# Kernel optimization log

Measured on AMD Instinct MI355X. Metric: run time of the kernel, lower is better.

The kernel has to match this reference:

```python
import jax, jax.numpy as jnp
import numpy as np

B = 262144
MF = 16  # metadata_features
C = 128  # trunk width
EPS = 1e-6


def _linear(x, w, b):
    # torch nn.Linear: y = x @ w.T + b, w shape [out, in]
    return x @ w.T + b


def _adain(x, style):
    # style: [B, 2*C] viewed as [B, C, 2]; [...,0]=scale, [...,1]=bias
    s = style.reshape(x.shape[0], x.shape[1], 2)
    scale, bias = s[:, :, 0], s[:, :, 1]
    mu = jnp.mean(x, axis=-1, keepdims=True)
    # torch.std default is unbiased (ddof=1)
    var = jnp.sum((x - mu) ** 2, axis=-1, keepdims=True) / (x.shape[1] - 1)
    sigma = jnp.sqrt(var) + EPS
    return scale * (x - mu) / sigma + bias


def setup_inputs() -> dict:
    key = jax.random.key(0)
    ks = jax.random.split(key, 20)
    n = jax.random.normal
    d = dict(
        x=n(ks[0], (B, 1), jnp.float32),
        metadata=n(ks[1], (B, MF), jnp.float32),
        # MetadataMLP: MF -> 64 -> 128 -> 1024
        mw1=n(ks[2], (64, MF), jnp.float32) * 0.2,
        mb1=jnp.zeros((64,), jnp.float32),
        mw2=n(ks[3], (128, 64), jnp.float32) * 0.1,
        mb2=jnp.zeros((128,), jnp.float32),
        mw3=n(ks[4], (1024, 128), jnp.float32) * 0.1,
        mb3=jnp.zeros((1024,), jnp.float32),
        # trunk
        w1=n(ks[5], (C, 1), jnp.float32) * 0.5,
        b1=jnp.zeros((C,), jnp.float32),
        w2=n(ks[6], (C, C), jnp.float32) * 0.1,
        b2=jnp.zeros((C,), jnp.float32),
        w3=n(ks[7], (C, C), jnp.float32) * 0.1,
        b3=jnp.zeros((C,), jnp.float32),
        w4=n(ks[8], (C, C), jnp.float32) * 0.1,
        b4=jnp.zeros((C,), jnp.float32),
        w5=n(ks[9], (1, C), jnp.float32) * 0.1,
        b5=jnp.zeros((1,), jnp.float32),
    )
    return d


def reference(x, metadata, mw1, mb1, mw2, mb2, mw3, mb3,
              w1, b1, w2, b2, w3, b3, w4, b4, w5, b5):
    lrelu = lambda v: jax.nn.leaky_relu(v, 0.01)
    # MetadataMLP -> style vectors [B, 1024]
    h = jax.nn.relu(_linear(metadata, mw1, mb1))
    h = jax.nn.relu(_linear(h, mw2, mb2))
    style = _linear(h, mw3, mb3)
    s1, s2, s3, s4 = jnp.split(style, 4, axis=1)  # each [B, 256]

    y = lrelu(_adain(_linear(x, w1, b1), s1))
    y = lrelu(_adain(_linear(y, w2, b2), s2))
    y = lrelu(_adain(_linear(y, w3, b3), s3))
    y = lrelu(_adain(_linear(y, w4, b4), s4))
    out = lrelu(_linear(y, w5, b5))  # [B, 1]
    return out
```

## Files before the change

### kernel.cpp

```cpp
#include <hip/hip_runtime.h>

#define RPB  64
#define NTHR 128

typedef _Float16 f16;
typedef _Float16 f16x4 __attribute__((ext_vector_type(4)));
typedef _Float16 f16x8 __attribute__((ext_vector_type(8)));
typedef float    f32x4 __attribute__((ext_vector_type(4)));

#define G_MW2 1024
#define G_W   2048
#define G_MW3 16384
#define GO_MW2 0
#define GO_W2  (GO_MW2 + G_MW2)
#define GO_W3  (GO_W2 + G_W)
#define GO_W4  (GO_W3 + G_W)
#define GO_MW3 (GO_W4 + G_W)
#define G_TOT  (GO_MW3 + G_MW3)
#define G_MW1Q 256
#define WS_BYTES ((size_t)G_TOT * 16 + (size_t)G_MW1Q * 8)

#define OFF_H2    0
#define OFF_B     17408
#define OFF_H1    (OFF_B)
#define OFF_STATS (OFF_B + 17408)
#define OFF_OUT   (OFF_STATS + 1024)
#define OFF_X     (OFF_OUT + 512)
#define SMEM_SZ   (OFF_X + 256)

__device__ __forceinline__ f16x8 cvt8(const float* __restrict__ p) {
  const float4* p4 = (const float4*)p;
  float4 f0 = p4[0], f1 = p4[1];
  f16x8 o;
  o[0]=(f16)f0.x; o[1]=(f16)f0.y; o[2]=(f16)f0.z; o[3]=(f16)f0.w;
  o[4]=(f16)f1.x; o[5]=(f16)f1.y; o[6]=(f16)f1.z; o[7]=(f16)f1.w;
  return o;
}

__device__ __forceinline__ f16x4 cvt4v(float4 f) {
  f16x4 o;
  o[0]=(f16)f.x; o[1]=(f16)f.y; o[2]=(f16)f.z; o[3]=(f16)f.w;
  return o;
}

__global__ void pack_weights(const float* __restrict__ mw1, const float* __restrict__ mw2,
                             const float* __restrict__ w2,  const float* __restrict__ w3,
                             const float* __restrict__ w4,  const float* __restrict__ mw3,
                             f16x8* __restrict__ ws) {
  int g = blockIdx.x * blockDim.x + threadIdx.x;
  if (g >= G_TOT + G_MW1Q) return;
  if (g >= G_TOT) {
    const int local = g - G_TOT;
    const int lane = local & 63, jt = local >> 6;
    const int j = jt * 16 + (lane & 15);
    const int k0 = (lane >> 4) * 4;
    ((f16x4*)(ws + G_TOT))[local] = cvt4v(*(const float4*)(mw1 + j * 16 + k0));
    return;
  }
  if (g < GO_MW3) {
    const float* W; int K; int local;
    if (g < GO_W2)       { W = mw2; K = 64;  local = g; }
    else if (g < GO_W3)  { W = w2;  K = 128; local = g - GO_W2; }
    else if (g < GO_W4)  { W = w3;  K = 128; local = g - GO_W3; }
    else                 { W = w4;  K = 128; local = g - GO_W4; }
    const int lane = local & 63, fb = local >> 6;
    const int ksteps = K >> 5;
    const int ks = fb % ksteps, n0g = fb / ksteps;
    const int n  = n0g * 16 + (lane & 15);
    const int k0 = ks * 32 + (lane >> 4) * 8;
    ws[g] = cvt8(W + (size_t)n * K + k0);
  } else {
    const int local = g - GO_MW3;
    const int lane = local & 63, fb = local >> 6;
    const int ks = fb & 3, sb = (fb >> 2) & 1, tt = (fb >> 3) & 3;
    const int ch = (fb >> 5) & 1, l = fb >> 6;
    const int n  = l * 256 + 2 * (ch * 64 + tt * 16 + (lane & 15)) + sb;
    const int k0 = ks * 32 + (lane >> 4) * 8;
    ws[g] = cvt8(mw3 + (size_t)n * 128 + k0);
  }
}

template<bool WS>
__device__ __forceinline__ f16x8 ldB(const f16x8* __restrict__ wp,
                                     const float* __restrict__ wf,
                                     int K, int n0, int ks, int lane) {
  if constexpr (WS) {
    return wp[((n0 >> 4) * (K >> 5) + ks) * 64 + lane];
  } else {
    const int n  = n0 + (lane & 15);
    const int k0 = ks * 32 + (lane >> 4) * 8;
    return cvt8(wf + (size_t)n * K + k0);
  }
}

template<bool WS>
__device__ __forceinline__ f16x8 ldB3(const f16x8* __restrict__ wp,
                                      const float* __restrict__ wf,
                                      int l, int ch, int tt, int sb, int ks, int lane) {
  if constexpr (WS) {
    const int fb = (((l * 2 + ch) * 4 + tt) * 2 + sb) * 4 + ks;
    return wp[fb * 64 + lane];
  } else {
    const int n  = l * 256 + 2 * (ch * 64 + tt * 16 + (lane & 15)) + sb;
    const int k0 = ks * 32 + (lane >> 4) * 8;
    return cvt8(wf + (size_t)n * 128 + k0);
  }
}

template<bool WS>
__device__ __forceinline__ f16x4 ldB1(const f16x8* __restrict__ wsp,
                                      const float* __restrict__ mw1f,
                                      int jt, int lane) {
  if constexpr (WS) {
    return ((const f16x4*)(wsp + G_TOT))[jt * 64 + lane];
  } else {
    const int j = jt * 16 + (lane & 15);
    const int k0 = (lane >> 4) * 4;
    return cvt4v(*(const float4*)(mw1f + j * 16 + k0));
  }
}

#define MFMA(a, b, c)   __builtin_amdgcn_mfma_f32_16x16x32_f16((a), (b), (c), 0, 0, 0)
#define MFMA16(a, b, c) __builtin_amdgcn_mfma_f32_16x16x16f16((a), (b), (c), 0, 0, 0)

template<bool WS>
__global__ __launch_bounds__(NTHR, 2)
void adain_mfma(const float* __restrict__ x,   const float* __restrict__ meta,
                const float* __restrict__ mw1, const float* __restrict__ mb1,
                const float* __restrict__ mw2, const float* __restrict__ mb2,
                const float* __restrict__ mw3, const float* __restrict__ mb3,
                const float* __restrict__ w1,  const float* __restrict__ b1,
                const float* __restrict__ w2,  const float* __restrict__ b2,
                const float* __restrict__ w3,  const float* __restrict__ b3,
                const float* __restrict__ w4,  const float* __restrict__ b4,
                const float* __restrict__ w5,  const float* __restrict__ b5,
                const f16x8* __restrict__ wsp, float* __restrict__ out)
{
  __shared__ __align__(16) char smem[SMEM_SZ];
  f16    (*sH2)[136]   = (f16(*)[136])  (smem + OFF_H2);
  f16    (*sH1)[72]    = (f16(*)[72])   (smem + OFF_H1);
  f16    (*sY)[136]    = (f16(*)[136])  (smem + OFF_B);
  float2 (*sStats)[2]  = (float2(*)[2]) (smem + OFF_STATS);
  float  (*sOut)[2]    = (float(*)[2])  (smem + OFF_OUT);
  float  *sX           = (float*)       (smem + OFF_X);

  const int t    = threadIdx.x;
  const int lane = t & 63;
  const int ch   = t >> 6;
  const int r0   = blockIdx.x * RPB;
  const int ln   = lane & 15;
  const int bg   = lane >> 4;
  const int acol = bg * 8;
  const int g4   = bg * 4;

  const f16x8* wsp3 = wsp + GO_MW3;

  if (t < RPB) sX[t] = x[r0 + t];

  {
    f16x4 am[4];
#pragma unroll
    for (int p = 0; p < 4; ++p)
      am[p] = cvt4v(*(const float4*)(meta + (size_t)(r0 + p * 16 + ln) * 16 + g4));
#pragma unroll
    for (int jj = 0; jj < 2; ++jj) {
      const int jt = ch * 2 + jj;
      const f16x4 wj = ldB1<WS>(wsp, mw1, jt, lane);
      const float4 bb = *(const float4*)(mb1 + jt * 16 + g4);
      const f32x4 cini = {bb.x, bb.y, bb.z, bb.w};
#pragma unroll
      for (int p = 0; p < 4; ++p) {
        f32x4 acc = MFMA16(wj, am[p], cini);
        f16x4 hv;
#pragma unroll
        for (int q = 0; q < 4; ++q) hv[q] = (f16)fmaxf(acc[q], 0.0f);
        *(f16x4*)&sH1[p * 16 + ln][jt * 16 + g4] = hv;
      }
    }
  }
  __syncthreads();

  {
    f16x8 a0[4], a1[4];
#pragma unroll
    for (int p = 0; p < 4; ++p) {
      const int ar = p * 16 + ln;
      a0[p] = *(const f16x8*)&sH1[ar][acol];
      a1[p] = *(const f16x8*)&sH1[ar][32 + acol];
    }
#pragma unroll
    for (int tt = 0; tt < 4; ++tt) {
      const int n0 = ch * 64 + tt * 16;
      f16x8 b0 = ldB<WS>(wsp + GO_MW2, mw2, 64, n0, 0, lane);
      f16x8 b1 = ldB<WS>(wsp + GO_MW2, mw2, 64, n0, 1, lane);
      const float4 bb = *(const float4*)(mb2 + n0 + g4);
      const f32x4 cini = {bb.x, bb.y, bb.z, bb.w};
#pragma unroll
      for (int p = 0; p < 4; ++p) {
        f32x4 acc = MFMA(b0, a0[p], cini);
        acc = MFMA(b1, a1[p], acc);
        f16x4 hv;
#pragma unroll
        for (int q = 0; q < 4; ++q) hv[q] = (f16)fmaxf(acc[q], 0.0f);
        *(f16x4*)&sH2[p * 16 + ln][n0 + g4] = hv;
      }
    }
  }
  __syncthreads();

#pragma unroll 1
  for (int l = 0; l < 4; ++l) {
    f32x4 accM[4][4];

    if (l == 0) {
#pragma unroll
      for (int tt = 0; tt < 4; ++tt) {
        const int c4 = ch * 64 + tt * 16 + g4;
        const float4 w1v = *(const float4*)(w1 + c4);
        const float4 b1v = *(const float4*)(b1 + c4);
#pragma unroll
        for (int p = 0; p < 4; ++p) {
          const float xv = sX[p * 16 + ln];
          accM[p][tt][0] = xv * w1v.x + b1v.x;
          accM[p][tt][1] = xv * w1v.y + b1v.y;
          accM[p][tt][2] = xv * w1v.z + b1v.z;
          accM[p][tt][3] = xv * w1v.w + b1v.w;
        }
      }
    } else {
      const f16x8* Wp_ = (l == 1) ? wsp + GO_W2 : (l == 2) ? wsp + GO_W3 : wsp + GO_W4;
      const float* Wf_ = (l == 1) ? w2 : (l == 2) ? w3 : w4;
      const float* Bv_ = (l == 1) ? b2 : (l == 2) ? b3 : b4;
#pragma unroll
      for (int tt = 0; tt < 4; ++tt) {
        const float4 bv = *(const float4*)(Bv_ + ch * 64 + tt * 16 + g4);
        const f32x4 cini = {bv.x, bv.y, bv.z, bv.w};
#pragma unroll
        for (int p = 0; p < 4; ++p)
          accM[p][tt] = cini;
      }
#pragma unroll
      for (int ks = 0; ks < 4; ++ks) {
        f16x8 aY[4];
#pragma unroll
        for (int p = 0; p < 4; ++p)
          aY[p] = *(const f16x8*)&sY[p * 16 + ln][ks * 32 + acol];
#pragma unroll
        for (int tt = 0; tt < 4; ++tt) {
          const f16x8 bm = ldB<WS>(Wp_, Wf_, 128, ch * 64 + tt * 16, ks, lane);
#pragma unroll
          for (int p = 0; p < 4; ++p)
            accM[p][tt] = MFMA(bm, aY[p], accM[p][tt]);
        }
      }
    }

    float s1[4] = {0,0,0,0}, s2[4] = {0,0,0,0};
#pragma unroll
    for (int p = 0; p < 4; ++p)
#pragma unroll
      for (int tt = 0; tt < 4; ++tt)
#pragma unroll
        for (int q = 0; q < 4; ++q) {
          const float v = accM[p][tt][q];
          s1[p] += v; s2[p] += v * v;
        }
#pragma unroll
    for (int p = 0; p < 4; ++p) {
      s1[p] += __shfl_xor(s1[p], 16, 64);
      s2[p] += __shfl_xor(s2[p], 16, 64);
      s1[p] += __shfl_xor(s1[p], 32, 64);
      s2[p] += __shfl_xor(s2[p], 32, 64);
    }
    if (lane < 16) {
#pragma unroll
      for (int p = 0; p < 4; ++p)
        sStats[p * 16 + ln][ch] = make_float2(s1[p], s2[p]);
    }
    __syncthreads();

#pragma unroll
    for (int p = 0; p < 4; ++p) {
      const int r = p * 16 + ln;
      const float2 A = sStats[r][0], Bc = sStats[r][1];
      const float S1 = A.x + Bc.x, S2 = A.y + Bc.y;
      const float m = S1 * (1.0f / 128.0f);
      float var = (S2 - S1 * m) * (1.0f / 127.0f);
      var = fmaxf(var, 0.0f);
      const float rsg = 1.0f / (sqrtf(var) + 1e-6f);
#pragma unroll
      for (int tt = 0; tt < 4; ++tt) {
        f16x4 zv;
#pragma unroll
        for (int q = 0; q < 4; ++q)
          zv[q] = (f16)((accM[p][tt][q] - m) * rsg);
        *(f16x4*)&sY[r][ch * 64 + tt * 16 + g4] = zv;
      }
    }

    f16x8 aH[4][4];
#pragma unroll
    for (int p = 0; p < 4; ++p) {
      const int ar = p * 16 + ln;
#pragma unroll
      for (int ks = 0; ks < 4; ++ks)
        aH[p][ks] = *(const f16x8*)&sH2[ar][ks * 32 + acol];
    }

    if (l < 3) {
#pragma unroll
      for (int tt = 0; tt < 4; ++tt) {
        const int c4 = ch * 64 + tt * 16 + g4;
        const float4 mv0 = *(const float4*)(mb3 + l * 256 + 2 * c4);
        const float4 mv1 = *(const float4*)(mb3 + l * 256 + 2 * c4 + 4);
        const f32x4 scI = {mv0.x, mv0.z, mv1.x, mv1.z};
        const f32x4 biI = {mv0.y, mv0.w, mv1.y, mv1.w};
        f32x4 sc[4], bi[4];
#pragma unroll
        for (int p = 0; p < 4; ++p) { sc[p] = scI; bi[p] = biI; }
#pragma unroll
        for (int ks = 0; ks < 4; ++ks) {
          const f16x8 bs0 = ldB3<WS>(wsp3, mw3, l, ch, tt, 0, ks, lane);
          const f16x8 bs1 = ldB3<WS>(wsp3, mw3, l, ch, tt, 1, ks, lane);
#pragma unroll
          for (int p = 0; p < 4; ++p) {
            sc[p] = MFMA(bs0, aH[p][ks], sc[p]);
            bi[p] = MFMA(bs1, aH[p][ks], bi[p]);
          }
        }
#pragma unroll
        for (int p = 0; p < 4; ++p) {
          const int r = p * 16 + ln;
          const f16x4 zv = *(const f16x4*)&sY[r][c4];
          f16x4 yv;
#pragma unroll
          for (int q = 0; q < 4; ++q) {
            float v = sc[p][q] * (float)zv[q] + bi[p][q];
            v = fmaxf(v, 0.01f * v);
            yv[q] = (f16)v;
          }
          *(f16x4*)&sY[r][c4] = yv;
        }
      }
      __syncthreads();
    } else {
      float o[4] = {0, 0, 0, 0};
#pragma unroll
      for (int tt = 0; tt < 4; ++tt) {
        const int c4 = ch * 64 + tt * 16 + g4;
        const float4 mv0 = *(const float4*)(mb3 + l * 256 + 2 * c4);
        const float4 mv1 = *(const float4*)(mb3 + l * 256 + 2 * c4 + 4);
        const f32x4 scI = {mv0.x, mv0.z, mv1.x, mv1.z};
        const f32x4 biI = {mv0.y, mv0.w, mv1.y, mv1.w};
        const float4 w5v = *(const float4*)(w5 + c4);
        const float w5q[4] = {w5v.x, w5v.y, w5v.z, w5v.w};
        f32x4 sc[4], bi[4];
#pragma unroll
        for (int p = 0; p < 4; ++p) { sc[p] = scI; bi[p] = biI; }
#pragma unroll
        for (int ks = 0; ks < 4; ++ks) {
          const f16x8 bs0 = ldB3<WS>(wsp3, mw3, l, ch, tt, 0, ks, lane);
          const f16x8 bs1 = ldB3<WS>(wsp3, mw3, l, ch, tt, 1, ks, lane);
#pragma unroll
          for (int p = 0; p < 4; ++p) {
            sc[p] = MFMA(bs0, aH[p][ks], sc[p]);
            bi[p] = MFMA(bs1, aH[p][ks], bi[p]);
          }
        }
#pragma unroll
        for (int p = 0; p < 4; ++p) {
          const f16x4 zv = *(const f16x4*)&sY[p * 16 + ln][c4];
#pragma unroll
          for (int q = 0; q < 4; ++q) {
            float v = sc[p][q] * (float)zv[q] + bi[p][q];
            v = fmaxf(v, 0.01f * v);
            o[p] += v * w5q[q];
          }
        }
      }
#pragma unroll
      for (int p = 0; p < 4; ++p) {
        o[p] += __shfl_xor(o[p], 16, 64);
        o[p] += __shfl_xor(o[p], 32, 64);
      }
      if (lane < 16) {
#pragma unroll
        for (int p = 0; p < 4; ++p)
          sOut[p * 16 + ln][ch] = o[p];
      }
      __syncthreads();
      if (t < RPB) {
        float v = sOut[t][0] + sOut[t][1] + b5[0];
        v = fmaxf(v, 0.01f * v);
        out[r0 + t] = v;
      }
    }
  }
}

extern "C" void kernel_launch(void* const* d_in, const int* in_sizes, int n_in,
                              void* d_out, int out_size, void* d_ws, size_t ws_size,
                              hipStream_t stream) {
  const float* x    = (const float*)d_in[0];
  const float* meta = (const float*)d_in[1];
  const float* mw1  = (const float*)d_in[2];
  const float* mb1  = (const float*)d_in[3];
  const float* mw2  = (const float*)d_in[4];
  const float* mb2  = (const float*)d_in[5];
  const float* mw3  = (const float*)d_in[6];
  const float* mb3  = (const float*)d_in[7];
  const float* w1   = (const float*)d_in[8];
  const float* b1   = (const float*)d_in[9];
  const float* w2   = (const float*)d_in[10];
  const float* b2   = (const float*)d_in[11];
  const float* w3   = (const float*)d_in[12];
  const float* b3   = (const float*)d_in[13];
  const float* w4   = (const float*)d_in[14];
  const float* b4   = (const float*)d_in[15];
  const float* w5   = (const float*)d_in[16];
  const float* b5   = (const float*)d_in[17];
  float* out = (float*)d_out;

  const int nrows = in_sizes[0];
  const int grid  = nrows / RPB;

  const bool usews = (ws_size >= WS_BYTES) && (d_ws != nullptr);
  if (usews) {
    f16x8* wsp = (f16x8*)d_ws;
    hipLaunchKernelGGL(pack_weights, dim3((G_TOT + G_MW1Q + 255) / 256), dim3(256), 0, stream,
                       mw1, mw2, w2, w3, w4, mw3, wsp);
    hipLaunchKernelGGL(adain_mfma<true>, dim3(grid), dim3(NTHR), 0, stream,
                       x, meta, mw1, mb1, mw2, mb2, mw3, mb3,
                       w1, b1, w2, b2, w3, b3, w4, b4, w5, b5, wsp, out);
  } else {
    hipLaunchKernelGGL(adain_mfma<false>, dim3(grid), dim3(NTHR), 0, stream,
                       x, meta, mw1, mb1, mw2, mb2, mw3, mb3,
                       w1, b1, w2, b2, w3, b3, w4, b4, w5, b5, (const f16x8*)nullptr, out);
  }
}
```

Baseline: 152.7 us.

## Double-buffer style and trunk weight fragments to prefetch ahead of MFMAs

Result: slower. 157.5 us (+3.1%).

```diff
diff --git a/kernel.cpp b/kernel.cpp
--- a/kernel.cpp
+++ b/kernel.cpp
@@ -123,6 +123,71 @@
 #define MFMA(a, b, c)   __builtin_amdgcn_mfma_f32_16x16x32_f16((a), (b), (c), 0, 0, 0)
 #define MFMA16(a, b, c) __builtin_amdgcn_mfma_f32_16x16x16f16((a), (b), (c), 0, 0, 0)
 
+#define LD_STYLE(B0, B1, L, TT) do {                                        \
+  _Pragma("unroll") for (int ks_ = 0; ks_ < 4; ++ks_) {                     \
+    B0[ks_] = ldB3<WS>(wsp3, mw3, (L), ch, (TT), 0, ks_, lane);             \
+    B1[ks_] = ldB3<WS>(wsp3, mw3, (L), ch, (TT), 1, ks_, lane);             \
+  } } while (0)
+
+#define STY_TT(B0, B1, TT) do {                                             \
+  const int c4_ = ch * 64 + (TT) * 16 + g4;                                 \
+  const float4 mv0_ = *(const float4*)(mb3 + l * 256 + 2 * c4_);            \
+  const float4 mv1_ = *(const float4*)(mb3 + l * 256 + 2 * c4_ + 4);        \
+  const f32x4 scI_ = {mv0_.x, mv0_.z, mv1_.x, mv1_.z};                      \
+  const f32x4 biI_ = {mv0_.y, mv0_.w, mv1_.y, mv1_.w};                      \
+  f32x4 sc_[4], bi_[4];                                                     \
+  _Pragma("unroll") for (int p_ = 0; p_ < 4; ++p_) { sc_[p_] = scI_; bi_[p_] = biI_; } \
+  _Pragma("unroll") for (int ks_ = 0; ks_ < 4; ++ks_)                       \
+    _Pragma("unroll") for (int p_ = 0; p_ < 4; ++p_) {                      \
+      sc_[p_] = MFMA(B0[ks_], aH[p_][ks_], sc_[p_]);                        \
+      bi_[p_] = MFMA(B1[ks_], aH[p_][ks_], bi_[p_]);                        \
+    }                                                                       \
+  _Pragma("unroll") for (int p_ = 0; p_ < 4; ++p_) {                        \
+    const int r_ = p_ * 16 + ln;                                            \
+    const f16x4 zv_ = *(const f16x4*)&sY[r_][c4_];                          \
+    f16x4 yv_;                                                              \
+    _Pragma("unroll") for (int q_ = 0; q_ < 4; ++q_) {                      \
+      float v_ = sc_[p_][q_] * (float)zv_[q_] + bi_[p_][q_];                \
+      v_ = fmaxf(v_, 0.01f * v_);                                           \
+      yv_[q_] = (f16)v_;                                                    \
+    }                                                                       \
+    *(f16x4*)&sY[r_][c4_] = yv_;                                            \
+  } } while (0)
+
+#define STY_TT_LAST(B0, B1, TT) do {                                        \
+  const int c4_ = ch * 64 + (TT) * 16 + g4;                                 \
+  const float4 mv0_ = *(const float4*)(mb3 + 3 * 256 + 2 * c4_);            \
+  const float4 mv1_ = *(const float4*)(mb3 + 3 * 256 + 2 * c4_ + 4);        \
+  const f32x4 scI_ = {mv0_.x, mv0_.z, mv1_.x, mv1_.z};                      \
+  const f32x4 biI_ = {mv0_.y, mv0_.w, mv1_.y, mv1_.w};                      \
+  const float4 w5v_ = *(const float4*)(w5 + c4_);                           \
+  const float w5q_[4] = {w5v_.x, w5v_.y, w5v_.z, w5v_.w};                   \
+  f32x4 sc_[4], bi_[4];                                                     \
+  _Pragma("unroll") for (int p_ = 0; p_ < 4; ++p_) { sc_[p_] = scI_; bi_[p_] = biI_; } \
+  _Pragma("unroll") for (int ks_ = 0; ks_ < 4; ++ks_)                       \
+    _Pragma("unroll") for (int p_ = 0; p_ < 4; ++p_) {                      \
+      sc_[p_] = MFMA(B0[ks_], aH[p_][ks_], sc_[p_]);                        \
+      bi_[p_] = MFMA(B1[ks_], aH[p_][ks_], bi_[p_]);                        \
+    }                                                                       \
+  _Pragma("unroll") for (int p_ = 0; p_ < 4; ++p_) {                        \
+    const f16x4 zv_ = *(const f16x4*)&sY[p_ * 16 + ln][c4_];                \
+    _Pragma("unroll") for (int q_ = 0; q_ < 4; ++q_) {                      \
+      float v_ = sc_[p_][q_] * (float)zv_[q_] + bi_[p_][q_];                \
+      v_ = fmaxf(v_, 0.01f * v_);                                           \
+      o[p_] += v_ * w5q_[q_];                                               \
+    }                                                                       \
+  } } while (0)
+
+#define LD_AY(BUF, KS) _Pragma("unroll") for (int p_ = 0; p_ < 4; ++p_)     \
+  BUF[p_] = *(const f16x8*)&sY[p_ * 16 + ln][(KS) * 32 + acol];
+
+#define LD_BM(BUF, KS) _Pragma("unroll") for (int tt_ = 0; tt_ < 4; ++tt_)  \
+  BUF[tt_] = ldB<WS>(Wp_, Wf_, 128, ch * 64 + tt_ * 16, (KS), lane);
+
+#define B_STEP(AYB, BMB) _Pragma("unroll") for (int tt_ = 0; tt_ < 4; ++tt_) \
+  _Pragma("unroll") for (int p_ = 0; p_ < 4; ++p_)                          \
+    accM[p_][tt_] = MFMA(BMB[tt_], AYB[p_], accM[p_][tt_]);
+
 template<bool WS>
 __global__ __launch_bounds__(NTHR, 2)
 void adain_mfma(const float* __restrict__ x,   const float* __restrict__ meta,
@@ -155,7 +220,11 @@
 
   const f16x8* wsp3 = wsp + GO_MW3;
 
+  f16x8 bsP0[4], bsP1[4], bsQ0[4], bsQ1[4];
+
   if (t < RPB) sX[t] = x[r0 + t];
+
+  LD_STYLE(bsP0, bsP1, 0, 0);
 
   {
     f16x4 am[4];
@@ -239,20 +308,15 @@
         for (int p = 0; p < 4; ++p)
           accM[p][tt] = cini;
       }
-#pragma unroll
-      for (int ks = 0; ks < 4; ++ks) {
-        f16x8 aY[4];
-#pragma unroll
-        for (int p = 0; p < 4; ++p)
-          aY[p] = *(const f16x8*)&sY[p * 16 + ln][ks * 32 + acol];
-#pragma unroll
-        for (int tt = 0; tt < 4; ++tt) {
-          const f16x8 bm = ldB<WS>(Wp_, Wf_, 128, ch * 64 + tt * 16, ks, lane);
-#pragma unroll
-          for (int p = 0; p < 4; ++p)
-            accM[p][tt] = MFMA(bm, aY[p], accM[p][tt]);
-        }
-      }
+      f16x8 aYA[4], aYB[4], bmA[4], bmB[4];
+      LD_AY(aYA, 0); LD_BM(bmA, 0);
+      LD_AY(aYB, 1); LD_BM(bmB, 1);
+      B_STEP(aYA, bmA);
+      LD_AY(aYA, 2); LD_BM(bmA, 2);
+      B_STEP(aYB, bmB);
+      LD_AY(aYB, 3); LD_BM(bmB, 3);
+      B_STEP(aYA, bmA);
+      B_STEP(aYB, bmB);
     }
 
     float s1[4] = {0,0,0,0}, s2[4] = {0,0,0,0};
@@ -277,6 +341,8 @@
       for (int p = 0; p < 4; ++p)
         sStats[p * 16 + ln][ch] = make_float2(s1[p], s2[p]);
     }
+
+    LD_STYLE(bsQ0, bsQ1, l, 1);
     __syncthreads();
 
 #pragma unroll
@@ -308,76 +374,22 @@
     }
 
     if (l < 3) {
-#pragma unroll
-      for (int tt = 0; tt < 4; ++tt) {
-        const int c4 = ch * 64 + tt * 16 + g4;
-        const float4 mv0 = *(const float4*)(mb3 + l * 256 + 2 * c4);
-        const float4 mv1 = *(const float4*)(mb3 + l * 256 + 2 * c4 + 4);
-        const f32x4 scI = {mv0.x, mv0.z, mv1.x, mv1.z};
-        const f32x4 biI = {mv0.y, mv0.w, mv1.y, mv1.w};
-        f32x4 sc[4], bi[4];
-#pragma unroll
-        for (int p = 0; p < 4; ++p) { sc[p] = scI; bi[p] = biI; }
-#pragma unroll
-        for (int ks = 0; ks < 4; ++ks) {
-          const f16x8 bs0 = ldB3<WS>(wsp3, mw3, l, ch, tt, 0, ks, lane);
-          const f16x8 bs1 = ldB3<WS>(wsp3, mw3, l, ch, tt, 1, ks, lane);
-#pragma unroll
-          for (int p = 0; p < 4; ++p) {
-            sc[p] = MFMA(bs0, aH[p][ks], sc[p]);
-            bi[p] = MFMA(bs1, aH[p][ks], bi[p]);
-          }
-        }
-#pragma unroll
-        for (int p = 0; p < 4; ++p) {
-          const int r = p * 16 + ln;
-          const f16x4 zv = *(const f16x4*)&sY[r][c4];
-          f16x4 yv;
-#pragma unroll
-          for (int q = 0; q < 4; ++q) {
-            float v = sc[p][q] * (float)zv[q] + bi[p][q];
-            v = fmaxf(v, 0.01f * v);
-            yv[q] = (f16)v;
-          }
-          *(f16x4*)&sY[r][c4] = yv;
-        }
-      }
+      STY_TT(bsP0, bsP1, 0);
+      LD_STYLE(bsP0, bsP1, l, 2);
+      STY_TT(bsQ0, bsQ1, 1);
+      LD_STYLE(bsQ0, bsQ1, l, 3);
+      STY_TT(bsP0, bsP1, 2);
+      LD_STYLE(bsP0, bsP1, l + 1, 0);
+      STY_TT(bsQ0, bsQ1, 3);
       __syncthreads();
     } else {
       float o[4] = {0, 0, 0, 0};
-#pragma unroll
-      for (int tt = 0; tt < 4; ++tt) {
-        const int c4 = ch * 64 + tt * 16 + g4;
-        const float4 mv0 = *(const float4*)(mb3 + l * 256 + 2 * c4);
-        const float4 mv1 = *(const float4*)(mb3 + l * 256 + 2 * c4 + 4);
-        const f32x4 scI = {mv0.x, mv0.z, mv1.x, mv1.z};
-        const f32x4 biI = {mv0.y, mv0.w, mv1.y, mv1.w};
-        const float4 w5v = *(const float4*)(w5 + c4);
-        const float w5q[4] = {w5v.x, w5v.y, w5v.z, w5v.w};
-        f32x4 sc[4], bi[4];
-#pragma unroll
-        for (int p = 0; p < 4; ++p) { sc[p] = scI; bi[p] = biI; }
-#pragma unroll
-        for (int ks = 0; ks < 4; ++ks) {
-          const f16x8 bs0 = ldB3<WS>(wsp3, mw3, l, ch, tt, 0, ks, lane);
-          const f16x8 bs1 = ldB3<WS>(wsp3, mw3, l, ch, tt, 1, ks, lane);
-#pragma unroll
-          for (int p = 0; p < 4; ++p) {
-            sc[p] = MFMA(bs0, aH[p][ks], sc[p]);
-            bi[p] = MFMA(bs1, aH[p][ks], bi[p]);
-          }
-        }
-#pragma unroll
-        for (int p = 0; p < 4; ++p) {
-          const f16x4 zv = *(const f16x4*)&sY[p * 16 + ln][c4];
-#pragma unroll
-          for (int q = 0; q < 4; ++q) {
-            float v = sc[p][q] * (float)zv[q] + bi[p][q];
-            v = fmaxf(v, 0.01f * v);
-            o[p] += v * w5q[q];
-          }
-        }
-      }
+      STY_TT_LAST(bsP0, bsP1, 0);
+      LD_STYLE(bsP0, bsP1, 3, 2);
+      STY_TT_LAST(bsQ0, bsQ1, 1);
+      LD_STYLE(bsQ0, bsQ1, 3, 3);
+      STY_TT_LAST(bsP0, bsP1, 2);
+      STY_TT_LAST(bsQ0, bsQ1, 3);
 #pragma unroll
       for (int p = 0; p < 4; ++p) {
         o[p] += __shfl_xor(o[p], 16, 64);
```

## Use single-wave blocks of 32 rows to drop cross-wave sync and stats exchange

Applied to the files above, without the earlier changes.

Result: slower. 245.3 us (+60.6%).

```diff
diff --git a/kernel.cpp b/kernel.cpp
--- a/kernel.cpp
+++ b/kernel.cpp
@@ -1,7 +1,7 @@
 #include <hip/hip_runtime.h>
 
-#define RPB  64
-#define NTHR 128
+#define RPB  32
+#define NTHR 64
 
 typedef _Float16 f16;
 typedef _Float16 f16x4 __attribute__((ext_vector_type(4)));
@@ -21,12 +21,10 @@
 #define WS_BYTES ((size_t)G_TOT * 16 + (size_t)G_MW1Q * 8)
 
 #define OFF_H2    0
-#define OFF_B     17408
+#define OFF_B     8704
 #define OFF_H1    (OFF_B)
-#define OFF_STATS (OFF_B + 17408)
-#define OFF_OUT   (OFF_STATS + 1024)
-#define OFF_X     (OFF_OUT + 512)
-#define SMEM_SZ   (OFF_X + 256)
+#define OFF_X     (OFF_B + 8704)
+#define SMEM_SZ   (OFF_X + 128)
 
 __device__ __forceinline__ f16x8 cvt8(const float* __restrict__ p) {
   const float4* p4 = (const float4*)p;
@@ -140,13 +138,9 @@
   f16    (*sH2)[136]   = (f16(*)[136])  (smem + OFF_H2);
   f16    (*sH1)[72]    = (f16(*)[72])   (smem + OFF_H1);
   f16    (*sY)[136]    = (f16(*)[136])  (smem + OFF_B);
-  float2 (*sStats)[2]  = (float2(*)[2]) (smem + OFF_STATS);
-  float  (*sOut)[2]    = (float(*)[2])  (smem + OFF_OUT);
   float  *sX           = (float*)       (smem + OFF_X);
 
-  const int t    = threadIdx.x;
-  const int lane = t & 63;
-  const int ch   = t >> 6;
+  const int lane = threadIdx.x;
   const int r0   = blockIdx.x * RPB;
   const int ln   = lane & 15;
   const int bg   = lane >> 4;
@@ -155,21 +149,20 @@
 
   const f16x8* wsp3 = wsp + GO_MW3;
 
-  if (t < RPB) sX[t] = x[r0 + t];
+  if (lane < RPB) sX[lane] = x[r0 + lane];
 
   {
-    f16x4 am[4];
-#pragma unroll
-    for (int p = 0; p < 4; ++p)
+    f16x4 am[2];
+#pragma unroll
+    for (int p = 0; p < 2; ++p)
       am[p] = cvt4v(*(const float4*)(meta + (size_t)(r0 + p * 16 + ln) * 16 + g4));
 #pragma unroll
-    for (int jj = 0; jj < 2; ++jj) {
-      const int jt = ch * 2 + jj;
+    for (int jt = 0; jt < 4; ++jt) {
       const f16x4 wj = ldB1<WS>(wsp, mw1, jt, lane);
       const float4 bb = *(const float4*)(mb1 + jt * 16 + g4);
       const f32x4 cini = {bb.x, bb.y, bb.z, bb.w};
 #pragma unroll
-      for (int p = 0; p < 4; ++p) {
+      for (int p = 0; p < 2; ++p) {
         f32x4 acc = MFMA16(wj, am[p], cini);
         f16x4 hv;
 #pragma unroll
@@ -178,25 +171,24 @@
       }
     }
   }
-  __syncthreads();
 
   {
-    f16x8 a0[4], a1[4];
-#pragma unroll
-    for (int p = 0; p < 4; ++p) {
+    f16x8 a0[2], a1[2];
+#pragma unroll
+    for (int p = 0; p < 2; ++p) {
       const int ar = p * 16 + ln;
       a0[p] = *(const f16x8*)&sH1[ar][acol];
       a1[p] = *(const f16x8*)&sH1[ar][32 + acol];
     }
 #pragma unroll
-    for (int tt = 0; tt < 4; ++tt) {
-      const int n0 = ch * 64 + tt * 16;
+    for (int tt = 0; tt < 8; ++tt) {
+      const int n0 = tt * 16;
       f16x8 b0 = ldB<WS>(wsp + GO_MW2, mw2, 64, n0, 0, lane);
       f16x8 b1 = ldB<WS>(wsp + GO_MW2, mw2, 64, n0, 1, lane);
       const float4 bb = *(const float4*)(mb2 + n0 + g4);
       const f32x4 cini = {bb.x, bb.y, bb.z, bb.w};
 #pragma unroll
-      for (int p = 0; p < 4; ++p) {
+      for (int p = 0; p < 2; ++p) {
         f32x4 acc = MFMA(b0, a0[p], cini);
         acc = MFMA(b1, a1[p], acc);
         f16x4 hv;
@@ -206,20 +198,19 @@
       }
     }
   }
-  __syncthreads();
 
 #pragma unroll 1
   for (int l = 0; l < 4; ++l) {
-    f32x4 accM[4][4];
+    f32x4 accM[2][8];
 
     if (l == 0) {
 #pragma unroll
-      for (int tt = 0; tt < 4; ++tt) {
-        const int c4 = ch * 64 + tt * 16 + g4;
+      for (int tt = 0; tt < 8; ++tt) {
+        const int c4 = tt * 16 + g4;
         const float4 w1v = *(const float4*)(w1 + c4);
         const float4 b1v = *(const float4*)(b1 + c4);
 #pragma unroll
-        for (int p = 0; p < 4; ++p) {
+        for (int p = 0; p < 2; ++p) {
           const float xv = sX[p * 16 + ln];
           accM[p][tt][0] = xv * w1v.x + b1v.x;
           accM[p][tt][1] = xv * w1v.y + b1v.y;
@@ -232,75 +223,67 @@
       const float* Wf_ = (l == 1) ? w2 : (l == 2) ? w3 : w4;
       const float* Bv_ = (l == 1) ? b2 : (l == 2) ? b3 : b4;
 #pragma unroll
-      for (int tt = 0; tt < 4; ++tt) {
-        const float4 bv = *(const float4*)(Bv_ + ch * 64 + tt * 16 + g4);
+      for (int tt = 0; tt < 8; ++tt) {
+        const float4 bv = *(const float4*)(Bv_ + tt * 16 + g4);
         const f32x4 cini = {bv.x, bv.y, bv.z, bv.w};
 #pragma unroll
-        for (int p = 0; p < 4; ++p)
+        for (int p = 0; p < 2; ++p)
           accM[p][tt] = cini;
       }
 #pragma unroll
       for (int ks = 0; ks < 4; ++ks) {
-        f16x8 aY[4];
-#pragma unroll
-        for (int p = 0; p < 4; ++p)
+        f16x8 aY[2];
+#pragma unroll
+        for (int p = 0; p < 2; ++p)
           aY[p] = *(const f16x8*)&sY[p * 16 + ln][ks * 32 + acol];
 #pragma unroll
-        for (int tt = 0; tt < 4; ++tt) {
-          const f16x8 bm = ldB<WS>(Wp_, Wf_, 128, ch * 64 + tt * 16, ks, lane);
-#pragma unroll
-          for (int p = 0; p < 4; ++p)
+        for (int tt = 0; tt < 8; ++tt) {
+          const f16x8 bm = ldB<WS>(Wp_, Wf_, 128, tt * 16, ks, lane);
+#pragma unroll
+          for (int p = 0; p < 2; ++p)
             accM[p][tt] = MFMA(bm, aY[p], accM[p][tt]);
         }
       }
     }
 
-    float s1[4] = {0,0,0,0}, s2[4] = {0,0,0,0};
-#pragma unroll
-    for (int p = 0; p < 4; ++p)
-#pragma unroll
-      for (int tt = 0; tt < 4; ++tt)
+    float s1[2] = {0, 0}, s2[2] = {0, 0};
+#pragma unroll
+    for (int p = 0; p < 2; ++p)
+#pragma unroll
+      for (int tt = 0; tt < 8; ++tt)
 #pragma unroll
         for (int q = 0; q < 4; ++q) {
           const float v = accM[p][tt][q];
           s1[p] += v; s2[p] += v * v;
         }
 #pragma unroll
-    for (int p = 0; p < 4; ++p) {
+    for (int p = 0; p < 2; ++p) {
       s1[p] += __shfl_xor(s1[p], 16, 64);
       s2[p] += __shfl_xor(s2[p], 16, 64);
       s1[p] += __shfl_xor(s1[p], 32, 64);
       s2[p] += __shfl_xor(s2[p], 32, 64);
     }
-    if (lane < 16) {
-#pragma unroll
-      for (int p = 0; p < 4; ++p)
-        sStats[p * 16 + ln][ch] = make_float2(s1[p], s2[p]);
-    }
-    __syncthreads();
-
-#pragma unroll
-    for (int p = 0; p < 4; ++p) {
+
+#pragma unroll
+    for (int p = 0; p < 2; ++p) {
       const int r = p * 16 + ln;
-      const float2 A = sStats[r][0], Bc = sStats[r][1];
-      const float S1 = A.x + Bc.x, S2 = A.y + Bc.y;
-      const float m = S1 * (1.0f / 128.0f);
-      float var = (S2 - S1 * m) * (1.0f / 127.0f);
+      const float m = s1[p] * (1.0f / 128.0f);
+      float var = (s2[p] - s1[p] * m) * (1.0f / 127.0f);
       var = fmaxf(var, 0.0f);
       const float rsg = 1.0f / (sqrtf(var) + 1e-6f);
 #pragma unroll
-      for (int tt = 0; tt < 4; ++tt) {
+      for (int tt = 0; tt < 8; ++tt) {
         f16x4 zv;
 #pragma unroll
         for (int q = 0; q < 4; ++q)
           zv[q] = (f16)((accM[p][tt][q] - m) * rsg);
-        *(f16x4*)&sY[r][ch * 64 + tt * 16 + g4] = zv;
-      }
-    }
-
-    f16x8 aH[4][4];
-#pragma unroll
-    for (int p = 0; p < 4; ++p) {
+        *(f16x4*)&sY[r][tt * 16 + g4] = zv;
+      }
+    }
+
+    f16x8 aH[2][4];
+#pragma unroll
+    for (int p = 0; p < 2; ++p) {
       const int ar = p * 16 + ln;
 #pragma unroll
       for (int ks = 0; ks < 4; ++ks)
@@ -309,27 +292,28 @@
 
     if (l < 3) {
 #pragma unroll
-      for (int tt = 0; tt < 4; ++tt) {
-        const int c4 = ch * 64 + tt * 16 + g4;
+      for (int tt = 0; tt < 8; ++tt) {
+        const int ch_ = tt >> 2, t3 = tt & 3;
+        const int c4 = tt * 16 + g4;
         const float4 mv0 = *(const float4*)(mb3 + l * 256 + 2 * c4);
         const float4 mv1 = *(const float4*)(mb3 + l * 256 + 2 * c4 + 4);
         const f32x4 scI = {mv0.x, mv0.z, mv1.x, mv1.z};
         const f32x4 biI = {mv0.y, mv0.w, mv1.y, mv1.w};
-        f32x4 sc[4], bi[4];
-#pragma unroll
-        for (int p = 0; p < 4; ++p) { sc[p] = scI; bi[p] = biI; }
+        f32x4 sc[2], bi[2];
+#pragma unroll
+        for (int p = 0; p < 2; ++p) { sc[p] = scI; bi[p] = biI; }
 #pragma unroll
         for (int ks = 0; ks < 4; ++ks) {
-          const f16x8 bs0 = ldB3<WS>(wsp3, mw3, l, ch, tt, 0, ks, lane);
-          const f16x8 bs1 = ldB3<WS>(wsp3, mw3, l, ch, tt, 1, ks, lane);
-#pragma unroll
-          for (int p = 0; p < 4; ++p) {
+          const f16x8 bs0 = ldB3<WS>(wsp3, mw3, l, ch_, t3, 0, ks, lane);
+          const f16x8 bs1 = ldB3<WS>(wsp3, mw3, l, ch_, t3, 1, ks, lane);
+#pragma unroll
+          for (int p = 0; p < 2; ++p) {
             sc[p] = MFMA(bs0, aH[p][ks], sc[p]);
             bi[p] = MFMA(bs1, aH[p][ks], bi[p]);
           }
         }
 #pragma unroll
-        for (int p = 0; p < 4; ++p) {
+        for (int p = 0; p < 2; ++p) {
           const int r = p * 16 + ln;
           const f16x4 zv = *(const f16x4*)&sY[r][c4];
           f16x4 yv;
@@ -342,33 +326,33 @@
           *(f16x4*)&sY[r][c4] = yv;
         }
       }
-      __syncthreads();
     } else {
-      float o[4] = {0, 0, 0, 0};
-#pragma unroll
-      for (int tt = 0; tt < 4; ++tt) {
-        const int c4 = ch * 64 + tt * 16 + g4;
+      float o[2] = {0, 0};
+#pragma unroll
+      for (int tt = 0; tt < 8; ++tt) {
+        const int ch_ = tt >> 2, t3 = tt & 3;
+        const int c4 = tt * 16 + g4;
         const float4 mv0 = *(const float4*)(mb3 + l * 256 + 2 * c4);
         const float4 mv1 = *(const float4*)(mb3 + l * 256 + 2 * c4 + 4);
         const f32x4 scI = {mv0.x, mv0.z, mv1.x, mv1.z};
         const f32x4 biI = {mv0.y, mv0.w, mv1.y, mv1.w};
         const float4 w5v = *(const float4*)(w5 + c4);
         const float w5q[4] = {w5v.x, w5v.y, w5v.z, w5v.w};
-        f32x4 sc[4], bi[4];
-#pragma unroll
-        for (int p = 0; p < 4; ++p) { sc[p] = scI; bi[p] = biI; }
+        f32x4 sc[2], bi[2];
+#pragma unroll
+        for (int p = 0; p < 2; ++p) { sc[p] = scI; bi[p] = biI; }
 #pragma unroll
         for (int ks = 0; ks < 4; ++ks) {
-          const f16x8 bs0 = ldB3<WS>(wsp3, mw3, l, ch, tt, 0, ks, lane);
-          const f16x8 bs1 = ldB3<WS>(wsp3, mw3, l, ch, tt, 1, ks, lane);
-#pragma unroll
-          for (int p = 0; p < 4; ++p) {
+          const f16x8 bs0 = ldB3<WS>(wsp3, mw3, l, ch_, t3, 0, ks, lane);
+          const f16x8 bs1 = ldB3<WS>(wsp3, mw3, l, ch_, t3, 1, ks, lane);
+#pragma unroll
+          for (int p = 0; p < 2; ++p) {
             sc[p] = MFMA(bs0, aH[p][ks], sc[p]);
             bi[p] = MFMA(bs1, aH[p][ks], bi[p]);
           }
         }
 #pragma unroll
-        for (int p = 0; p < 4; ++p) {
+        for (int p = 0; p < 2; ++p) {
           const f16x4 zv = *(const f16x4*)&sY[p * 16 + ln][c4];
 #pragma unroll
           for (int q = 0; q < 4; ++q) {
@@ -379,20 +363,17 @@
         }
       }
 #pragma unroll
-      for (int p = 0; p < 4; ++p) {
+      for (int p = 0; p < 2; ++p) {
         o[p] += __shfl_xor(o[p], 16, 64);
         o[p] += __shfl_xor(o[p], 32, 64);
       }
       if (lane < 16) {
 #pragma unroll
-        for (int p = 0; p < 4; ++p)
-          sOut[p * 16 + ln][ch] = o[p];
-      }
-      __syncthreads();
-      if (t < RPB) {
-        float v = sOut[t][0] + sOut[t][1] + b5[0];
-        v = fmaxf(v, 0.01f * v);
-        out[r0 + t] = v;
+        for (int p = 0; p < 2; ++p) {
+          float v = o[p] + b5[0];
+          v = fmaxf(v, 0.01f * v);
+          out[r0 + p * 16 + ln] = v;
+        }
       }
     }
   }
```
